# Performance work log

Measured on AMD Instinct MI355X. Metric: run time of the kernel, lower is better.

Reference implementation:

```python
import jax, jax.numpy as jnp
import numpy as np

EMBED_DIM = 512
NUM_HEADS = 8
HEAD_DIM = EMBED_DIM // NUM_HEADS


def setup_inputs() -> dict:
    key = jax.random.key(0)
    ks = jax.random.split(key, 6)
    B, S, E = 2, 4096, EMBED_DIM
    scale = 1.0 / np.sqrt(E)
    return {
        "rotation_params": jax.random.normal(ks[0], (E, E), jnp.float32) * scale,
        "entangle_params": jax.random.normal(ks[1], (E, E), jnp.float32) * scale,
        "inputs": jax.random.normal(ks[2], (B, S, E), jnp.float32),
        "w_q": jax.random.normal(ks[3], (E, E), jnp.float32) * scale,
        "w_k": jax.random.normal(ks[4], (E, E), jnp.float32) * scale,
        "w_v": jax.random.normal(ks[5], (E, E), jnp.float32) * scale,
    }


def reference(rotation_params, entangle_params, inputs, w_q, w_k, w_v):
    B, S, E = inputs.shape
    H, D = NUM_HEADS, HEAD_DIM
    # torch nn.Linear(x) = x @ W.T ; then extra matmul with rotation/entangle mats
    q = (inputs @ w_q.T) @ rotation_params  # [B,S,E]
    k = (inputs @ w_k.T) @ entangle_params  # [B,S,E]
    v = inputs @ w_v.T                       # [B,S,E]
    # split heads -> [B,H,S,D]
    q = q.reshape(B, S, H, D).transpose(0, 2, 1, 3)
    k = k.reshape(B, S, H, D).transpose(0, 2, 1, 3)
    v = v.reshape(B, S, H, D).transpose(0, 2, 1, 3)
    scores = jnp.einsum("bhqd,bhkd->bhqk", q, k) / jnp.sqrt(jnp.float32(D))
    attn = jax.nn.softmax(scores, axis=-1)  # dropout p=0 (eval) -> identity
    out = jnp.einsum("bhqk,bhkd->bhqd", attn, v)
    return out.transpose(0, 2, 1, 3).reshape(B, S, E)
```

## Files before the change

kernel.cpp:

```cpp
#include <hip/hip_runtime.h>
#include <cstddef>

#define E 512
#define H 8
#define D 64
#define BATCH 2
#define SEQ 4096

typedef __attribute__((ext_vector_type(8))) short bf16x8;
typedef __attribute__((ext_vector_type(4))) float f32x4;
typedef __attribute__((ext_vector_type(16))) float f32x16;
typedef __attribute__((ext_vector_type(4))) unsigned uint4v;

__device__ __forceinline__ ushort f2bf(float f) {
  unsigned u = __builtin_bit_cast(unsigned, f);
  u += 0x7fff + ((u >> 16) & 1);
  return (ushort)(u >> 16);
}
__device__ __forceinline__ float bf2f(ushort h) {
  return __builtin_bit_cast(float, (unsigned)h << 16);
}
__device__ __forceinline__ unsigned pk_bf16(float lo, float hi) {
#if __has_builtin(__builtin_amdgcn_cvt_pk_bf16_f32)
  typedef __attribute__((ext_vector_type(2))) __bf16 bfv2;
  bfv2 r = __builtin_amdgcn_cvt_pk_bf16_f32(lo, hi);
  return __builtin_bit_cast(unsigned, r);
#else
  return (unsigned)f2bf(lo) | ((unsigned)f2bf(hi) << 16);
#endif
}
__device__ __forceinline__ float fexp2(float x) {
#if __has_builtin(__builtin_amdgcn_exp2f)
  return __builtin_amdgcn_exp2f(x);
#else
  return exp2f(x);
#endif
}
__device__ __forceinline__ void permswap32(unsigned& a, unsigned& b) {
  asm("v_permlane32_swap_b32 %0, %1" : "+v"(a), "+v"(b));
}

__global__ __launch_bounds__(256) void xcast(const float* __restrict__ x,
                                             ushort* __restrict__ xh,
                                             ushort* __restrict__ xl) {
  size_t i = ((size_t)blockIdx.x * 256 + threadIdx.x) * 4;
  float4 v = *(const float4*)&x[i];
  ushort4 h, l;
  h.x = f2bf(v.x); l.x = f2bf(v.x - bf2f(h.x));
  h.y = f2bf(v.y); l.y = f2bf(v.y - bf2f(h.y));
  h.z = f2bf(v.z); l.z = f2bf(v.z - bf2f(h.z));
  h.w = f2bf(v.w); l.w = f2bf(v.w - bf2f(h.w));
  *(ushort4*)&xh[i] = h;
  *(ushort4*)&xl[i] = l;
}

__global__ __launch_bounds__(256) void fold_tiled(
    const float* __restrict__ wq, const float* __restrict__ wk,
    const float* __restrict__ rot, const float* __restrict__ ent,
    ushort* __restrict__ weffbT) {
  const int which = blockIdx.z;
  const float* w = which ? wk : wq;
  const float* r = which ? ent : rot;
  const int k = blockIdx.x * 256 + threadIdx.x;
  const int n0 = blockIdx.y * 8;
  float acc[8] = {};
  for (int j0 = 0; j0 < E; j0 += 16) {
    float wv_[16];
#pragma unroll
    for (int u = 0; u < 16; ++u) wv_[u] = w[(size_t)(j0 + u) * E + k];
#pragma unroll
    for (int u = 0; u < 16; ++u)
#pragma unroll
      for (int t = 0; t < 8; ++t)
        acc[t] += wv_[u] * r[(size_t)(j0 + u) * E + n0 + t];
  }
#pragma unroll
  for (int t = 0; t < 8; ++t)
    weffbT[(size_t)which * E * E + (size_t)(n0 + t) * E + k] = f2bf(acc[t]);
}

__global__ __launch_bounds__(256) void wv_cast(const float* __restrict__ wv,
                                               ushort* __restrict__ dst) {
  size_t i = ((size_t)blockIdx.x * 256 + threadIdx.x) * 4;
  float4 v = *(const float4*)&wv[i];
  ushort4 o;
  o.x = f2bf(v.x); o.y = f2bf(v.y); o.z = f2bf(v.z); o.w = f2bf(v.w);
  *(ushort4*)&dst[i] = o;
}

#define LDA 40

__global__ __launch_bounds__(256) void qkv_fused(
    const ushort* __restrict__ xhg, const ushort* __restrict__ xlg,
    const ushort* __restrict__ weffbT, ushort* __restrict__ qg,
    ushort* __restrict__ kg, ushort* __restrict__ vtg) {
  __shared__ ushort sm[5 * 64 * LDA];
  ushort* Ah = sm;
  ushort* Al = sm + 64 * LDA;
  ushort* Bs = sm + 2 * 64 * LDA;
  ushort* vt_tile = Bs;

  const int head = blockIdx.x;
  const int m0 = blockIdx.y * 64;
  const int tid = threadIdx.x;
  const int wave = tid >> 6, lane = tid & 63;
  const int l15 = lane & 15, quad = lane >> 4;
  const int ar = tid >> 2, ac8 = (tid & 3) * 8;

  const ushort* arow = xhg + (size_t)(m0 + ar) * E + ac8;
  const ushort* lrow = xlg + (size_t)(m0 + ar) * E + ac8;
  const ushort* b0row = weffbT + (size_t)(head * 64 + ar) * E + ac8;

  f32x4 acc[3][4];
#pragma unroll
  for (int w = 0; w < 3; ++w)
#pragma unroll
    for (int nt = 0; nt < 4; ++nt) acc[w][nt] = (f32x4){0.f, 0.f, 0.f, 0.f};

  uint4 pa_h = *(const uint4*)&arow[0];
  uint4 pa_l = *(const uint4*)&lrow[0];
  uint4 pb0 = *(const uint4*)&b0row[0];
  uint4 pb1 = *(const uint4*)&b0row[E * E];
  uint4 pb2 = *(const uint4*)&b0row[2 * E * E];

  for (int k0 = 0; k0 < E; k0 += 32) {
    __syncthreads();
    *(uint4*)&Ah[ar * LDA + ac8] = pa_h;
    *(uint4*)&Al[ar * LDA + ac8] = pa_l;
    *(uint4*)&Bs[0 * 64 * LDA + ar * LDA + ac8] = pb0;
    *(uint4*)&Bs[1 * 64 * LDA + ar * LDA + ac8] = pb1;
    *(uint4*)&Bs[2 * 64 * LDA + ar * LDA + ac8] = pb2;
    __syncthreads();

    const int kn = (k0 + 32 < E) ? k0 + 32 : 0;
    pa_h = *(const uint4*)&arow[kn];
    pa_l = *(const uint4*)&lrow[kn];
    pb0 = *(const uint4*)&b0row[kn];
    pb1 = *(const uint4*)&b0row[E * E + kn];
    pb2 = *(const uint4*)&b0row[2 * E * E + kn];

    bf16x8 ah = *(const bf16x8*)&Ah[(wave * 16 + l15) * LDA + quad * 8];
    bf16x8 al = *(const bf16x8*)&Al[(wave * 16 + l15) * LDA + quad * 8];
#pragma unroll
    for (int w = 0; w < 3; ++w)
#pragma unroll
      for (int nt = 0; nt < 4; ++nt) {
        bf16x8 bf = *(const bf16x8*)&Bs[w * 64 * LDA + (nt * 16 + l15) * LDA +
                                        quad * 8];
        acc[w][nt] =
            __builtin_amdgcn_mfma_f32_16x16x32_bf16(ah, bf, acc[w][nt], 0, 0, 0);
        acc[w][nt] =
            __builtin_amdgcn_mfma_f32_16x16x32_bf16(al, bf, acc[w][nt], 0, 0, 0);
      }
  }

  const int b = m0 >> 12;
  const int s_base = m0 & (SEQ - 1);
  const float QSCALE = 0.125f * 1.44269504f;

#pragma unroll
  for (int w = 0; w < 2; ++w) {
    ushort* dst = (w == 0) ? qg : kg;
    float sc = (w == 0) ? QSCALE : 1.0f;
#pragma unroll
    for (int nt = 0; nt < 4; ++nt)
#pragma unroll
      for (int r = 0; r < 4; ++r) {
        float v = acc[w][nt][r] * sc;
        float vo = __shfl_xor(v, 1);
        if (!(lane & 1)) {
          int s = s_base + wave * 16 + quad * 4 + r;
          size_t ix = ((size_t)(b * H + head) * SEQ + s) * D + nt * 16 + l15;
          *(unsigned*)&dst[ix] = pk_bf16(v, vo);
        }
      }
  }

  __syncthreads();
#pragma unroll
  for (int nt = 0; nt < 4; ++nt) {
    uint2 w2;
    w2.x = pk_bf16(acc[2][nt][0], acc[2][nt][1]);
    w2.y = pk_bf16(acc[2][nt][2], acc[2][nt][3]);
    *(uint2*)&vt_tile[(nt * 16 + l15) * 72 + wave * 16 + quad * 4] = w2;
  }
  __syncthreads();
  {
    int vr = tid >> 2, vs = (tid & 3) * 16;
    uint4 c0 = *(const uint4*)&vt_tile[vr * 72 + vs];
    uint4 c1 = *(const uint4*)&vt_tile[vr * 72 + vs + 8];
    size_t vo = ((size_t)(b * H + head) * D + vr) * SEQ + s_base + vs;
    *(uint4*)&vtg[vo] = c0;
    *(uint4*)&vtg[vo + 8] = c1;
  }
}

#define LDK 72

__global__ __launch_bounds__(256, 2) void attn_mfma(
    const ushort* __restrict__ qg, const ushort* __restrict__ kg,
    const ushort* __restrict__ vtg, float* __restrict__ out) {
  __shared__ ushort Ks[64 * LDK];
  __shared__ ushort Vs[64 * LDK];

  const int qt = blockIdx.x;
  const int bh = blockIdx.y;
  const int tid = threadIdx.x;
  const int wave = tid >> 6;
  const int lane = tid & 63;
  const int l31 = lane & 31, hi = lane >> 5;

  const ushort* qp = qg + (size_t)bh * SEQ * D;
  const ushort* kp = kg + (size_t)bh * SEQ * D;
  const ushort* vp = vtg + (size_t)bh * D * SEQ;

  const int qrow0 = qt * 128 + wave * 32;
  bf16x8 qf[4];
#pragma unroll
  for (int ds = 0; ds < 4; ++ds)
    qf[ds] =
        *(const bf16x8*)&qp[(size_t)(qrow0 + l31) * D + ds * 16 + hi * 8];

  f32x16 o[2];
  o[0] = 0.f;
  o[1] = 0.f;
  float l_r = 0.f;

  const int r0 = tid >> 3, c0 = (tid & 7) * 8;
  const int r1 = 32 + r0;

  uint4 pk0 = *(const uint4*)&kp[(size_t)r0 * D + c0];
  uint4 pk1 = *(const uint4*)&kp[(size_t)r1 * D + c0];
  uint4 pv0 = *(const uint4*)&vp[(size_t)r0 * SEQ + c0];
  uint4 pv1 = *(const uint4*)&vp[(size_t)r1 * SEQ + c0];

  for (int it = 0; it < SEQ / 64; ++it) {
    __syncthreads();
    *(uint4*)&Ks[r0 * LDK + c0] = pk0;
    *(uint4*)&Ks[r1 * LDK + c0] = pk1;
    *(uint4*)&Vs[r0 * LDK + c0] = pv0;
    *(uint4*)&Vs[r1 * LDK + c0] = pv1;
    __syncthreads();

    {
      const int itn = (it + 1 < SEQ / 64) ? it + 1 : it;
      const ushort* ksrc = kp + (size_t)itn * 64 * D;
      pk0 = *(const uint4*)&ksrc[r0 * D + c0];
      pk1 = *(const uint4*)&ksrc[r1 * D + c0];
      pv0 = *(const uint4*)&vp[(size_t)r0 * SEQ + itn * 64 + c0];
      pv1 = *(const uint4*)&vp[(size_t)r1 * SEQ + itn * 64 + c0];
    }

    __builtin_amdgcn_s_setprio(1);
    f32x16 st0 = 0.f, st1 = 0.f;
#pragma unroll
    for (int ds = 0; ds < 4; ++ds) {
      bf16x8 kf0 = *(const bf16x8*)&Ks[(l31)*LDK + ds * 16 + hi * 8];
      bf16x8 kf1 = *(const bf16x8*)&Ks[(32 + l31) * LDK + ds * 16 + hi * 8];
      st0 = __builtin_amdgcn_mfma_f32_32x32x16_bf16(kf0, qf[ds], st0, 0, 0, 0);
      st1 = __builtin_amdgcn_mfma_f32_32x32x16_bf16(kf1, qf[ds], st1, 0, 0, 0);
    }

    bf16x8 pf00, pf01;
    {
      float pv[16];
#pragma unroll
      for (int r = 0; r < 16; ++r) pv[r] = fexp2(st0[r]);
      float s01 = (pv[0] + pv[1]) + (pv[2] + pv[3]);
      float s23 = (pv[4] + pv[5]) + (pv[6] + pv[7]);
      float s45 = (pv[8] + pv[9]) + (pv[10] + pv[11]);
      float s67 = (pv[12] + pv[13]) + (pv[14] + pv[15]);
      l_r += (s01 + s23) + (s45 + s67);
      unsigned w0[4], w1[4];
#pragma unroll
      for (int j = 0; j < 2; ++j) {
        {
          unsigned c0w = pk_bf16(pv[2 * j + 0], pv[2 * j + 1]);
          unsigned c1w = pk_bf16(pv[2 * j + 4], pv[2 * j + 5]);
          permswap32(c0w, c1w);
          w0[j] = c0w;
          w0[2 + j] = c1w;
        }
        {
          unsigned c0w = pk_bf16(pv[2 * j + 8], pv[2 * j + 9]);
          unsigned c1w = pk_bf16(pv[2 * j + 12], pv[2 * j + 13]);
          permswap32(c0w, c1w);
          w1[j] = c0w;
          w1[2 + j] = c1w;
        }
      }
      pf00 = __builtin_bit_cast(bf16x8, (uint4v){w0[0], w0[1], w0[2], w0[3]});
      pf01 = __builtin_bit_cast(bf16x8, (uint4v){w1[0], w1[1], w1[2], w1[3]});
    }
#pragma unroll
    for (int nt = 0; nt < 2; ++nt) {
      bf16x8 vf0 = *(const bf16x8*)&Vs[(nt * 32 + l31) * LDK + hi * 8];
      o[nt] =
          __builtin_amdgcn_mfma_f32_32x32x16_bf16(pf00, vf0, o[nt], 0, 0, 0);
      bf16x8 vf1 = *(const bf16x8*)&Vs[(nt * 32 + l31) * LDK + 16 + hi * 8];
      o[nt] =
          __builtin_amdgcn_mfma_f32_32x32x16_bf16(pf01, vf1, o[nt], 0, 0, 0);
    }

    bf16x8 pf10, pf11;
    {
      float pv[16];
#pragma unroll
      for (int r = 0; r < 16; ++r) pv[r] = fexp2(st1[r]);
      float s01 = (pv[0] + pv[1]) + (pv[2] + pv[3]);
      float s23 = (pv[4] + pv[5]) + (pv[6] + pv[7]);
      float s45 = (pv[8] + pv[9]) + (pv[10] + pv[11]);
      float s67 = (pv[12] + pv[13]) + (pv[14] + pv[15]);
      l_r += (s01 + s23) + (s45 + s67);
      unsigned w0[4], w1[4];
#pragma unroll
      for (int j = 0; j < 2; ++j) {
        {
          unsigned c0w = pk_bf16(pv[2 * j + 0], pv[2 * j + 1]);
          unsigned c1w = pk_bf16(pv[2 * j + 4], pv[2 * j + 5]);
          permswap32(c0w, c1w);
          w0[j] = c0w;
          w0[2 + j] = c1w;
        }
        {
          unsigned c0w = pk_bf16(pv[2 * j + 8], pv[2 * j + 9]);
          unsigned c1w = pk_bf16(pv[2 * j + 12], pv[2 * j + 13]);
          permswap32(c0w, c1w);
          w1[j] = c0w;
          w1[2 + j] = c1w;
        }
      }
      pf10 = __builtin_bit_cast(bf16x8, (uint4v){w0[0], w0[1], w0[2], w0[3]});
      pf11 = __builtin_bit_cast(bf16x8, (uint4v){w1[0], w1[1], w1[2], w1[3]});
    }
#pragma unroll
    for (int nt = 0; nt < 2; ++nt) {
      bf16x8 vf0 = *(const bf16x8*)&Vs[(nt * 32 + l31) * LDK + 32 + hi * 8];
      o[nt] =
          __builtin_amdgcn_mfma_f32_32x32x16_bf16(pf10, vf0, o[nt], 0, 0, 0);
      bf16x8 vf1 = *(const bf16x8*)&Vs[(nt * 32 + l31) * LDK + 48 + hi * 8];
      o[nt] =
          __builtin_amdgcn_mfma_f32_32x32x16_bf16(pf11, vf1, o[nt], 0, 0, 0);
    }
    __builtin_amdgcn_s_setprio(0);
  }

  float lg = l_r + __shfl_xor(l_r, 32);
  float linv = 1.f / lg;
  const int b = bh >> 3, h = bh & 7;
#pragma unroll
  for (int r = 0; r < 16; ++r) {
    int row = (r & 3) + 8 * (r >> 2) + 4 * hi;
    float inv = __shfl(linv, row);
    int srow = qt * 128 + wave * 32 + row;
#pragma unroll
    for (int nt = 0; nt < 2; ++nt) {
      out[((size_t)b * SEQ + srow) * E + h * D + nt * 32 + l31] =
          o[nt][r] * inv;
    }
  }
}

extern "C" void kernel_launch(void* const* d_in, const int* in_sizes, int n_in,
                              void* d_out, int out_size, void* d_ws,
                              size_t ws_size, hipStream_t stream) {
  const float* rot = (const float*)d_in[0];
  const float* ent = (const float*)d_in[1];
  const float* x = (const float*)d_in[2];
  const float* wq = (const float*)d_in[3];
  const float* wk = (const float*)d_in[4];
  const float* wv = (const float*)d_in[5];
  float* out = (float*)d_out;

  const size_t NX = (size_t)BATCH * SEQ * E;
  ushort* weffbT = (ushort*)d_ws;
  ushort* xh = weffbT + 3 * E * E;
  ushort* xl = xh + NX;
  ushort* qg = xl + NX;
  ushort* kg = qg + NX;
  ushort* vtg = kg + NX;

  xcast<<<dim3(NX / 1024), 256, 0, stream>>>(x, xh, xl);
  fold_tiled<<<dim3(E / 256, E / 8, 2), 256, 0, stream>>>(wq, wk, rot, ent,
                                                          weffbT);
  wv_cast<<<dim3(E * E / 1024), 256, 0, stream>>>(wv, weffbT + 2 * E * E);
  qkv_fused<<<dim3(H, BATCH * SEQ / 64), 256, 0, stream>>>(xh, xl, weffbT, qg,
                                                           kg, vtg);
  attn_mfma<<<dim3(SEQ / 128, BATCH * H), 256, 0, stream>>>(qg, kg, vtg, out);
}
```

Baseline: 246.6 us.

## Split attention key range across two wave groups per block and merge outputs

Doubles the attention block to 512 threads, with two groups of four waves that each handle alternate 64-key tiles for the same 128 query rows. The partial outputs and row sums from group 1 are passed through shared memory and added into group 0 before normalisation and the store. The aim is more waves per CU and better latency hiding on a grid of only 512 blocks. The cost is a larger shared-memory footprint, an extra reduction and sync at the end, and a 4-blocks-per-CU launch bound that may limit registers. The softmax has no max subtraction, so the partial sums can be added directly.

```diff
diff --git a/kernel.cpp b/kernel.cpp
--- a/kernel.cpp
+++ b/kernel.cpp
@@ -197,24 +197,30 @@
 
 #define LDK 72
 
-__global__ __launch_bounds__(256, 2) void attn_mfma(
+__global__ __launch_bounds__(512, 4) void attn_mfma(
     const ushort* __restrict__ qg, const ushort* __restrict__ kg,
     const ushort* __restrict__ vtg, float* __restrict__ out) {
-  __shared__ ushort Ks[64 * LDK];
-  __shared__ ushort Vs[64 * LDK];
+  __shared__ ushort sm[4 * 64 * LDK + 256];
+  ushort* Ks0 = sm;
+  ushort* Vs0 = sm + 2 * 64 * LDK;
+  float* lex = (float*)(sm + 4 * 64 * LDK);
 
   const int qt = blockIdx.x;
   const int bh = blockIdx.y;
   const int tid = threadIdx.x;
   const int wave = tid >> 6;
+  const int grp = wave >> 2, wq = wave & 3;
   const int lane = tid & 63;
   const int l31 = lane & 31, hi = lane >> 5;
+  const int gtid = tid & 255;
 
   const ushort* qp = qg + (size_t)bh * SEQ * D;
   const ushort* kp = kg + (size_t)bh * SEQ * D;
   const ushort* vp = vtg + (size_t)bh * D * SEQ;
-
-  const int qrow0 = qt * 128 + wave * 32;
+  ushort* Ksg = Ks0 + grp * 64 * LDK;
+  ushort* Vsg = Vs0 + grp * 64 * LDK;
+
+  const int qrow0 = qt * 128 + wq * 32;
   bf16x8 qf[4];
 #pragma unroll
   for (int ds = 0; ds < 4; ++ds)
@@ -226,37 +232,38 @@
   o[1] = 0.f;
   float l_r = 0.f;
 
-  const int r0 = tid >> 3, c0 = (tid & 7) * 8;
+  const int r0 = gtid >> 3, c0 = (gtid & 7) * 8;
   const int r1 = 32 + r0;
 
-  uint4 pk0 = *(const uint4*)&kp[(size_t)r0 * D + c0];
-  uint4 pk1 = *(const uint4*)&kp[(size_t)r1 * D + c0];
-  uint4 pv0 = *(const uint4*)&vp[(size_t)r0 * SEQ + c0];
-  uint4 pv1 = *(const uint4*)&vp[(size_t)r1 * SEQ + c0];
-
-  for (int it = 0; it < SEQ / 64; ++it) {
+  uint4 pk0 = *(const uint4*)&kp[(size_t)(grp * 64 + r0) * D + c0];
+  uint4 pk1 = *(const uint4*)&kp[(size_t)(grp * 64 + r1) * D + c0];
+  uint4 pv0 = *(const uint4*)&vp[(size_t)r0 * SEQ + grp * 64 + c0];
+  uint4 pv1 = *(const uint4*)&vp[(size_t)r1 * SEQ + grp * 64 + c0];
+
+  for (int it = 0; it < SEQ / 128; ++it) {
     __syncthreads();
-    *(uint4*)&Ks[r0 * LDK + c0] = pk0;
-    *(uint4*)&Ks[r1 * LDK + c0] = pk1;
-    *(uint4*)&Vs[r0 * LDK + c0] = pv0;
-    *(uint4*)&Vs[r1 * LDK + c0] = pv1;
+    *(uint4*)&Ksg[r0 * LDK + c0] = pk0;
+    *(uint4*)&Ksg[r1 * LDK + c0] = pk1;
+    *(uint4*)&Vsg[r0 * LDK + c0] = pv0;
+    *(uint4*)&Vsg[r1 * LDK + c0] = pv1;
     __syncthreads();
 
     {
-      const int itn = (it + 1 < SEQ / 64) ? it + 1 : it;
-      const ushort* ksrc = kp + (size_t)itn * 64 * D;
+      const int itn = (it + 1 < SEQ / 128) ? it + 1 : it;
+      const int ktn = itn * 2 + grp;
+      const ushort* ksrc = kp + (size_t)ktn * 64 * D;
       pk0 = *(const uint4*)&ksrc[r0 * D + c0];
       pk1 = *(const uint4*)&ksrc[r1 * D + c0];
-      pv0 = *(const uint4*)&vp[(size_t)r0 * SEQ + itn * 64 + c0];
-      pv1 = *(const uint4*)&vp[(size_t)r1 * SEQ + itn * 64 + c0];
+      pv0 = *(const uint4*)&vp[(size_t)r0 * SEQ + ktn * 64 + c0];
+      pv1 = *(const uint4*)&vp[(size_t)r1 * SEQ + ktn * 64 + c0];
     }
 
     __builtin_amdgcn_s_setprio(1);
     f32x16 st0 = 0.f, st1 = 0.f;
 #pragma unroll
     for (int ds = 0; ds < 4; ++ds) {
-      bf16x8 kf0 = *(const bf16x8*)&Ks[(l31)*LDK + ds * 16 + hi * 8];
-      bf16x8 kf1 = *(const bf16x8*)&Ks[(32 + l31) * LDK + ds * 16 + hi * 8];
+      bf16x8 kf0 = *(const bf16x8*)&Ksg[(l31)*LDK + ds * 16 + hi * 8];
+      bf16x8 kf1 = *(const bf16x8*)&Ksg[(32 + l31) * LDK + ds * 16 + hi * 8];
       st0 = __builtin_amdgcn_mfma_f32_32x32x16_bf16(kf0, qf[ds], st0, 0, 0, 0);
       st1 = __builtin_amdgcn_mfma_f32_32x32x16_bf16(kf1, qf[ds], st1, 0, 0, 0);
     }
@@ -294,10 +301,10 @@
     }
 #pragma unroll
     for (int nt = 0; nt < 2; ++nt) {
-      bf16x8 vf0 = *(const bf16x8*)&Vs[(nt * 32 + l31) * LDK + hi * 8];
+      bf16x8 vf0 = *(const bf16x8*)&Vsg[(nt * 32 + l31) * LDK + hi * 8];
       o[nt] =
           __builtin_amdgcn_mfma_f32_32x32x16_bf16(pf00, vf0, o[nt], 0, 0, 0);
-      bf16x8 vf1 = *(const bf16x8*)&Vs[(nt * 32 + l31) * LDK + 16 + hi * 8];
+      bf16x8 vf1 = *(const bf16x8*)&Vsg[(nt * 32 + l31) * LDK + 16 + hi * 8];
       o[nt] =
           __builtin_amdgcn_mfma_f32_32x32x16_bf16(pf01, vf1, o[nt], 0, 0, 0);
     }
@@ -335,28 +342,43 @@
     }
 #pragma unroll
     for (int nt = 0; nt < 2; ++nt) {
-      bf16x8 vf0 = *(const bf16x8*)&Vs[(nt * 32 + l31) * LDK + 32 + hi * 8];
+      bf16x8 vf0 = *(const bf16x8*)&Vsg[(nt * 32 + l31) * LDK + 32 + hi * 8];
       o[nt] =
           __builtin_amdgcn_mfma_f32_32x32x16_bf16(pf10, vf0, o[nt], 0, 0, 0);
-      bf16x8 vf1 = *(const bf16x8*)&Vs[(nt * 32 + l31) * LDK + 48 + hi * 8];
+      bf16x8 vf1 = *(const bf16x8*)&Vsg[(nt * 32 + l31) * LDK + 48 + hi * 8];
       o[nt] =
           __builtin_amdgcn_mfma_f32_32x32x16_bf16(pf11, vf1, o[nt], 0, 0, 0);
     }
     __builtin_amdgcn_s_setprio(0);
   }
 
+  __syncthreads();
   float lg = l_r + __shfl_xor(l_r, 32);
-  float linv = 1.f / lg;
-  const int b = bh >> 3, h = bh & 7;
-#pragma unroll
-  for (int r = 0; r < 16; ++r) {
-    int row = (r & 3) + 8 * (r >> 2) + 4 * hi;
-    float inv = __shfl(linv, row);
-    int srow = qt * 128 + wave * 32 + row;
-#pragma unroll
-    for (int nt = 0; nt < 2; ++nt) {
-      out[((size_t)b * SEQ + srow) * E + h * D + nt * 32 + l31] =
-          o[nt][r] * inv;
+  float* Oex = (float*)sm;
+  if (grp == 1) {
+#pragma unroll
+    for (int nt = 0; nt < 2; ++nt)
+#pragma unroll
+      for (int r = 0; r < 16; ++r) {
+        int row = (r & 3) + 8 * (r >> 2) + 4 * hi;
+        Oex[(wq * 32 + row) * 68 + nt * 32 + l31] = o[nt][r];
+      }
+    if (lane < 32) lex[wq * 32 + l31] = lg;
+  }
+  __syncthreads();
+  if (grp == 0) {
+    float linv = 1.f / (lg + lex[wq * 32 + l31]);
+    const int b = bh >> 3, h = bh & 7;
+#pragma unroll
+    for (int r = 0; r < 16; ++r) {
+      int row = (r & 3) + 8 * (r >> 2) + 4 * hi;
+      float inv = __shfl(linv, row);
+      int srow = qt * 128 + wq * 32 + row;
+#pragma unroll
+      for (int nt = 0; nt < 2; ++nt) {
+        float val = o[nt][r] + Oex[(wq * 32 + row) * 68 + nt * 32 + l31];
+        out[((size_t)b * SEQ + srow) * E + h * D + nt * 32 + l31] = val * inv;
+      }
     }
   }
 }
@@ -386,5 +408,5 @@
   wv_cast<<<dim3(E * E / 1024), 256, 0, stream>>>(wv, weffbT + 2 * E * E);
   qkv_fused<<<dim3(H, BATCH * SEQ / 64), 256, 0, stream>>>(xh, xl, weffbT, qg,
                                                            kg, vtg);
-  attn_mfma<<<dim3(SEQ / 128, BATCH * H), 256, 0, stream>>>(qg, kg, vtg, out);
-}
+  attn_mfma<<<dim3(SEQ / 128, BATCH * H), 512, 0, stream>>>(qg, kg, vtg, out);
+}
```

Result: slower. 263.0 us (+6.6%).
